# Performance work log

Measured on AMD Instinct MI355X. Metric: run time of the kernel, lower is better.

Reference implementation:

```python
import jax, jax.numpy as jnp
import numpy as np

# --- config (matches init_kwargs) ---
D_MODEL = 512
N_HEADS = 8
DIM_HEAD = D_MODEL // N_HEADS  # 64
BUCKET_SIZE = 64
N_HASHES = 4
B = 4
N = 4096
SELF_ATTN_VALUE = -5e4  # TOKEN_SELF_ATTN_VALUE in reformer_pytorch


def setup_inputs() -> dict:
    key = jax.random.key(0)
    ks = jax.random.split(key, 8)
    n_buckets = N // BUCKET_SIZE
    dh = N_HEADS * DIM_HEAD
    return {
        "queries": jax.random.normal(ks[0], (B, N, D_MODEL), jnp.float32),
        "keys": jax.random.normal(ks[1], (B, N, D_MODEL), jnp.float32),      # unused by module
        "values": jax.random.normal(ks[2], (B, N, D_MODEL), jnp.float32),    # unused by module
        "W_qk": jax.random.normal(ks[3], (D_MODEL, dh), jnp.float32) / np.float32(np.sqrt(D_MODEL)),
        "W_v": jax.random.normal(ks[4], (D_MODEL, dh), jnp.float32) / np.float32(np.sqrt(D_MODEL)),
        "W_out": jax.random.normal(ks[5], (dh, D_MODEL), jnp.float32) / np.float32(np.sqrt(dh)),
        "b_out": jnp.zeros((D_MODEL,), jnp.float32),
        # random LSH rotations: generated fresh (non-learnable) in torch; fixed here for determinism
        "rotations": jax.random.normal(ks[6], (DIM_HEAD, N_HASHES, n_buckets // 2), jnp.float32),
    }


def _look_one_back(x):
    # concat each chunk with the previous chunk along the within-chunk axis
    return jnp.concatenate([x, jnp.roll(x, 1, axis=1)], axis=2)


def lsh_attention(qk, v, rotations):
    # qk, v: (BH, T, dh) shared-QK LSH attention (reformer_pytorch LSHAttention)
    bh, T, dh = qk.shape
    n_buckets = T // BUCKET_SIZE
    total = N_HASHES * T

    # --- hash_vectors: random rotations + argmax over [R, -R] ---
    rotated = jnp.einsum('btf,fhi->bhti', qk, rotations)          # (bh, n_hashes, T, nb/2)
    rotated = jnp.concatenate([rotated, -rotated], axis=-1)       # (bh, n_hashes, T, nb)
    buckets = jnp.argmax(rotated, axis=-1)                        # (bh, n_hashes, T)
    offsets = (jnp.arange(N_HASHES) * n_buckets)[None, :, None]
    buckets = (buckets + offsets).reshape(bh, total)

    # --- stable sort by (bucket, position); keys are unique ---
    ticker = jnp.broadcast_to(jnp.arange(total)[None, :], (bh, total))
    buckets_and_t = T * buckets + (ticker % T)
    sticker = jnp.argsort(buckets_and_t, axis=-1)                 # (bh, total)
    undo_sort = jnp.argsort(sticker, axis=-1)
    st = sticker % T                                              # original positions, sorted

    sqk = jnp.take_along_axis(qk, st[:, :, None], axis=1)         # (bh, total, dh)
    sv = jnp.take_along_axis(v, st[:, :, None], axis=1)

    # --- chunk into bins; attend within chunk + one chunk back ---
    chunks = N_HASHES * n_buckets                                 # per-chunk len == BUCKET_SIZE
    bq_t = st.reshape(bh, chunks, -1)
    bqk = sqk.reshape(bh, chunks, -1, dh)
    bv = sv.reshape(bh, chunks, -1, dh)

    bq = bqk
    bk = bqk / jnp.maximum(jnp.linalg.norm(bqk, axis=-1, keepdims=True), 1e-12)  # F.normalize

    bk = _look_one_back(bk)       # (bh, chunks, 2*bs, dh)
    bv = _look_one_back(bv)
    bkv_t = _look_one_back(bq_t)  # (bh, chunks, 2*bs)

    dots = jnp.einsum('bcie,bcje->bcij', bq, bk) * (dh ** -0.5)   # (bh, chunks, bs, 2*bs)
    self_mask = bq_t[:, :, :, None] == bkv_t[:, :, None, :]
    dots = jnp.where(self_mask, SELF_ATTN_VALUE, dots)

    lse = jax.scipy.special.logsumexp(dots, axis=-1, keepdims=True)
    probs = jnp.exp(dots - lse)
    bo = jnp.einsum('bcij,bcje->bcie', probs, bv)                 # (bh, chunks, bs, dh)

    so = bo.reshape(bh, total, dh)
    slogits = lse.reshape(bh, total)
    o = jnp.take_along_axis(so, undo_sort[:, :, None], axis=1)
    logits = jnp.take_along_axis(slogits, undo_sort, axis=1)

    o = o.reshape(bh, N_HASHES, T, dh)
    logits = logits.reshape(bh, N_HASHES, T, 1)
    # combine hash rounds by softmax over per-round logsumexps
    w = jnp.exp(logits - jax.scipy.special.logsumexp(logits, axis=1, keepdims=True))
    return jnp.sum(o * w, axis=1)                                 # (bh, T, dh)


def reference(queries, keys, values, W_qk, W_v, W_out, b_out, rotations):
    Bsz, T, _ = queries.shape
    qk = queries @ W_qk                                           # (B, T, H*dh), no bias
    v = queries @ W_v

    def merge(x):
        return x.reshape(Bsz, T, N_HEADS, DIM_HEAD).transpose(0, 2, 1, 3).reshape(Bsz * N_HEADS, T, DIM_HEAD)

    out = lsh_attention(merge(qk), merge(v), rotations)           # (B*H, T, dh)
    out = out.reshape(Bsz, N_HEADS, T, DIM_HEAD).transpose(0, 2, 1, 3).reshape(Bsz, T, N_HEADS * DIM_HEAD)
    return out @ W_out + b_out                                    # to_out (with bias)
```

## Files before the change

### kernel.cpp

```cpp
#include <hip/hip_runtime.h>

typedef unsigned int uint32;
typedef _Float16 f16;
typedef _Float16 f16x8 __attribute__((ext_vector_type(8)));
typedef float f32x4 __attribute__((ext_vector_type(4)));

#define B_SZ 4
#define T_SZ 4096
#define DMODEL 512
#define NHEAD 8
#define DH 64
#define NHASH 4
#define BH (B_SZ*NHEAD)
#define NBUCK 256
#define TOT (NHASH*T_SZ)
#define M_TOK (B_SZ*T_SZ)

#define KSTRIDE 72
#define PSTRIDE 136

#define AMB_TAU 1.5e-3f

__global__ void k0_zero(int* hist, int* amb_cnt){
  hist[blockIdx.x*256 + threadIdx.x] = 0;
  if (blockIdx.x == 0 && threadIdx.x == 0) *amb_cnt = 0;
}

__global__ __launch_bounds__(256) void kw_t(const float* __restrict__ Wqk,
    const float* __restrict__ Wv, const float* __restrict__ Wout,
    f16* __restrict__ Wth, f16* __restrict__ Wtl)
{
  int gid = blockIdx.x*256 + threadIdx.x;
  int n = gid >> 9, k = gid & 511;
  int sel = n >> 9, col = n & 511;
  const float* src = (sel==0)? Wqk : (sel==1)? Wv : Wout;
  float v = src[(size_t)k*512 + col];
  f16 h = (f16)v;
  Wth[gid] = h;
  Wtl[gid] = (f16)(v - (float)h);
}

__global__ __launch_bounds__(256) void kr_t(const float* __restrict__ rot,
    f16* __restrict__ rotTh, f16* __restrict__ rotTl)
{
  int gid = blockIdx.x*256 + threadIdx.x;
  int n = gid >> 6, dd = gid & 63;
  float v = rot[dd*128 + n];
  f16 h = (f16)v;
  rotTh[gid] = h;
  rotTl[gid] = (f16)(v - (float)h);
}

__global__ __launch_bounds__(256) void k1a_split(const float* __restrict__ qin,
    f16* __restrict__ Ah, f16* __restrict__ Al)
{
  size_t gid = (size_t)blockIdx.x*256 + threadIdx.x;
  const float4* src = (const float4*)(qin) + gid*2;
  float4 x0 = src[0], x1 = src[1];
  float v[8] = {x0.x,x0.y,x0.z,x0.w, x1.x,x1.y,x1.z,x1.w};
  f16x8 h, l;
  #pragma unroll
  for (int e=0;e<8;e++){ f16 hh=(f16)v[e]; h[e]=hh; l[e]=(f16)(v[e]-(float)hh); }
  ((f16x8*)Ah)[gid] = h;
  ((f16x8*)Al)[gid] = l;
}

__global__ __launch_bounds__(256) void g_qkv(const f16* __restrict__ Ah,
    const f16* __restrict__ Al, const f16* __restrict__ Wth, const f16* __restrict__ Wtl,
    f16* __restrict__ qk16, f16* __restrict__ qkl, f16* __restrict__ v16)
{
  __shared__ f16 ah[128*KSTRIDE], al[128*KSTRIDE], bh[128*KSTRIDE], bl[128*KSTRIDE];
  int tid = threadIdx.x;
  int m0 = blockIdx.x*128, n0 = blockIdx.y*128;
  int w = tid >> 6, lane = tid & 63;
  int wm = w >> 1, wn = w & 1;
  int c_lane = lane & 15, quad = lane >> 4;

  f32x4 acc[4][4];
  #pragma unroll
  for (int mi=0;mi<4;mi++)
    #pragma unroll
    for (int ni=0;ni<4;ni++) acc[mi][ni] = (f32x4){0.f,0.f,0.f,0.f};

  int sr = tid >> 1, sc = (tid & 1) * 32;
  for (int kc=0; kc<8; kc++){
    int k0 = kc*64;
    {
      const f16x8* pah = (const f16x8*)(Ah + (size_t)(m0+sr)*512 + k0 + sc);
      const f16x8* pal = (const f16x8*)(Al + (size_t)(m0+sr)*512 + k0 + sc);
      const f16x8* pbh = (const f16x8*)(Wth + (size_t)(n0+sr)*512 + k0 + sc);
      const f16x8* pbl = (const f16x8*)(Wtl + (size_t)(n0+sr)*512 + k0 + sc);
      f16x8* dah = (f16x8*)&ah[sr*KSTRIDE + sc];
      f16x8* dal = (f16x8*)&al[sr*KSTRIDE + sc];
      f16x8* dbh = (f16x8*)&bh[sr*KSTRIDE + sc];
      f16x8* dbl = (f16x8*)&bl[sr*KSTRIDE + sc];
      #pragma unroll
      for (int i=0;i<4;i++){ dah[i]=pah[i]; dal[i]=pal[i]; dbh[i]=pbh[i]; dbl[i]=pbl[i]; }
    }
    __syncthreads();
    f16x8 fah[4][2], fal[4][2], fbh[4][2], fbl[4][2];
    #pragma unroll
    for (int i=0;i<4;i++)
      #pragma unroll
      for (int kb=0;kb<2;kb++){
        int ma = (wm*64 + i*16 + c_lane)*KSTRIDE + kb*32 + quad*8;
        int nb = (wn*64 + i*16 + c_lane)*KSTRIDE + kb*32 + quad*8;
        fah[i][kb] = *(const f16x8*)&ah[ma];
        fal[i][kb] = *(const f16x8*)&al[ma];
        fbh[i][kb] = *(const f16x8*)&bh[nb];
        fbl[i][kb] = *(const f16x8*)&bl[nb];
      }
    #pragma unroll
    for (int kb=0;kb<2;kb++)
      #pragma unroll
      for (int p=0;p<3;p++)
        #pragma unroll
        for (int mi=0;mi<4;mi++)
          #pragma unroll
          for (int ni=0;ni<4;ni++){
            f16x8 a = (p==2)? fal[mi][kb] : fah[mi][kb];
            f16x8 b = (p==1)? fbl[ni][kb] : fbh[ni][kb];
            acc[mi][ni] = __builtin_amdgcn_mfma_f32_16x16x32_f16(a, b, acc[mi][ni], 0,0,0);
          }
    __syncthreads();
  }

  #pragma unroll
  for (int mi=0;mi<4;mi++)
    #pragma unroll
    for (int ni=0;ni<4;ni++)
      #pragma unroll
      for (int r=0;r<4;r++){
        int n = n0 + wn*64 + ni*16 + c_lane;
        int tok = m0 + wm*64 + mi*16 + quad*4 + r;
        float val = acc[mi][ni][r];
        int b = tok >> 12, tp = tok & 4095;
        if (n < 512){
          int head = n >> 6, dd = n & 63;
          size_t idx = ((size_t)(b*NHEAD+head)*T_SZ + tp)*DH + dd;
          f16 hv = (f16)val;
          qk16[idx] = hv;
          qkl[idx]  = (f16)(val - (float)hv);
        } else {
          int j = n - 512, head = j >> 6, dd = j & 63;
          size_t idx = ((size_t)(b*NHEAD+head)*T_SZ + tp)*DH + dd;
          v16[idx] = (f16)val;
        }
      }
}

__global__ __launch_bounds__(256) void g_out(const f16* __restrict__ Xh,
    const f16* __restrict__ Xl, const f16* __restrict__ Wth, const f16* __restrict__ Wtl,
    const float* __restrict__ bout, float* __restrict__ out)
{
  __shared__ f16 ah[128*KSTRIDE], al[128*KSTRIDE], bh[128*KSTRIDE], bl[128*KSTRIDE];
  int tid = threadIdx.x;
  int m0 = blockIdx.x*128, n0 = blockIdx.y*128;
  int w = tid >> 6, lane = tid & 63;
  int wm = w >> 1, wn = w & 1;
  int c_lane = lane & 15, quad = lane >> 4;
  const f16* Bh_base = Wth + (size_t)1024*512;
  const f16* Bl_base = Wtl + (size_t)1024*512;

  f32x4 acc[4][4];
  #pragma unroll
  for (int mi=0;mi<4;mi++)
    #pragma unroll
    for (int ni=0;ni<4;ni++) acc[mi][ni] = (f32x4){0.f,0.f,0.f,0.f};

  int sr = tid >> 1, sc = (tid & 1) * 32;
  for (int kc=0; kc<8; kc++){
    int k0 = kc*64;
    {
      const f16x8* pah = (const f16x8*)(Xh + (size_t)(m0+sr)*512 + k0 + sc);
      const f16x8* pal = (const f16x8*)(Xl + (size_t)(m0+sr)*512 + k0 + sc);
      const f16x8* pbh = (const f16x8*)(Bh_base + (size_t)(n0+sr)*512 + k0 + sc);
      const f16x8* pbl = (const f16x8*)(Bl_base + (size_t)(n0+sr)*512 + k0 + sc);
      f16x8* dah = (f16x8*)&ah[sr*KSTRIDE + sc];
      f16x8* dal = (f16x8*)&al[sr*KSTRIDE + sc];
      f16x8* dbh = (f16x8*)&bh[sr*KSTRIDE + sc];
      f16x8* dbl = (f16x8*)&bl[sr*KSTRIDE + sc];
      #pragma unroll
      for (int i=0;i<4;i++){ dah[i]=pah[i]; dal[i]=pal[i]; dbh[i]=pbh[i]; dbl[i]=pbl[i]; }
    }
    __syncthreads();
    f16x8 fah[4][2], fal[4][2], fbh[4][2], fbl[4][2];
    #pragma unroll
    for (int i=0;i<4;i++)
      #pragma unroll
      for (int kb=0;kb<2;kb++){
        int ma = (wm*64 + i*16 + c_lane)*KSTRIDE + kb*32 + quad*8;
        int nb = (wn*64 + i*16 + c_lane)*KSTRIDE + kb*32 + quad*8;
        fah[i][kb] = *(const f16x8*)&ah[ma];
        fal[i][kb] = *(const f16x8*)&al[ma];
        fbh[i][kb] = *(const f16x8*)&bh[nb];
        fbl[i][kb] = *(const f16x8*)&bl[nb];
      }
    #pragma unroll
    for (int kb=0;kb<2;kb++)
      #pragma unroll
      for (int p=0;p<3;p++)
        #pragma unroll
        for (int mi=0;mi<4;mi++)
          #pragma unroll
          for (int ni=0;ni<4;ni++){
            f16x8 a = (p==2)? fal[mi][kb] : fah[mi][kb];
            f16x8 b = (p==1)? fbl[ni][kb] : fbh[ni][kb];
            acc[mi][ni] = __builtin_amdgcn_mfma_f32_16x16x32_f16(a, b, acc[mi][ni], 0,0,0);
          }
    __syncthreads();
  }

  #pragma unroll
  for (int mi=0;mi<4;mi++)
    #pragma unroll
    for (int ni=0;ni<4;ni++){
      int n = n0 + wn*64 + ni*16 + c_lane;
      float bn = bout[n];
      #pragma unroll
      for (int r=0;r<4;r++){
        int tok = m0 + wm*64 + mi*16 + quad*4 + r;
        out[(size_t)tok*512 + n] = acc[mi][ni][r] + bn;
      }
    }
}

__global__ __launch_bounds__(256) void k2_mfma(const f16* __restrict__ qkh,
    const f16* __restrict__ qkl, const f16* __restrict__ rotTh, const f16* __restrict__ rotTl,
    unsigned short* __restrict__ bucket, int* __restrict__ hist,
    int* __restrict__ amb_list, int* __restrict__ amb_cnt)
{
  int tid = threadIdx.x;
  int w = tid >> 6, lane = tid & 63;
  int wm = w >> 1, wn = w & 1;
  int c_lane = lane & 15, quad = lane >> 4;
  size_t m0 = (size_t)blockIdx.x*128 + wm*64;

  f16x8 fbh[4][2], fbl[4][2];
  #pragma unroll
  for (int ni=0;ni<4;ni++)
    #pragma unroll
    for (int kb=0;kb<2;kb++){
      int n = wn*64 + ni*16 + c_lane;
      fbh[ni][kb] = *(const f16x8*)&rotTh[n*64 + kb*32 + quad*8];
      fbl[ni][kb] = *(const f16x8*)&rotTl[n*64 + kb*32 + quad*8];
    }

  f32x4 acc[4][4];
  #pragma unroll
  for (int mi=0;mi<4;mi++)
    #pragma unroll
    for (int ni=0;ni<4;ni++) acc[mi][ni] = (f32x4){0.f,0.f,0.f,0.f};

  #pragma unroll
  for (int mi=0;mi<4;mi++){
    size_t row = m0 + mi*16 + c_lane;
    f16x8 fah[2], fal[2];
    #pragma unroll
    for (int kb=0;kb<2;kb++){
      fah[kb] = *(const f16x8*)&qkh[row*64 + kb*32 + quad*8];
      fal[kb] = *(const f16x8*)&qkl[row*64 + kb*32 + quad*8];
    }
    #pragma unroll
    for (int kb=0;kb<2;kb++)
      #pragma unroll
      for (int ni=0;ni<4;ni++){
        acc[mi][ni] = __builtin_amdgcn_mfma_f32_16x16x32_f16(fah[kb], fbh[ni][kb], acc[mi][ni], 0,0,0);
        acc[mi][ni] = __builtin_amdgcn_mfma_f32_16x16x32_f16(fah[kb], fbl[ni][kb], acc[mi][ni], 0,0,0);
        acc[mi][ni] = __builtin_amdgcn_mfma_f32_16x16x32_f16(fal[kb], fbh[ni][kb], acc[mi][ni], 0,0,0);
      }
  }

  #pragma unroll
  for (int mi=0;mi<4;mi++){
    #pragma unroll
    for (int r=0;r<4;r++){
      int tok = (int)m0 + mi*16 + quad*4 + r;
      int bhh = tok >> 12, t = tok & 4095;
      #pragma unroll
      for (int hl=0; hl<2; hl++){
        int h = wn*2 + hl;
        float v0 = acc[mi][2*hl][r];
        float v1 = acc[mi][2*hl+1][r];
        float m1 = v0, m2 = -1e30f; int b1 = c_lane;
        if (v1 > m1){ m2 = m1; m1 = v1; b1 = 16 + c_lane; } else m2 = v1;
        float n0v = -v0, n1v = -v1;
        if (n0v > m1){ m2 = m1; m1 = n0v; b1 = 32 + c_lane; } else if (n0v > m2) m2 = n0v;
        if (n1v > m1){ m2 = m1; m1 = n1v; b1 = 48 + c_lane; } else if (n1v > m2) m2 = n1v;
        float ssq = v0*v0 + v1*v1;
        #pragma unroll
        for (int d2=1; d2<16; d2<<=1){
          float om1 = __shfl_xor(m1, d2);
          float om2 = __shfl_xor(m2, d2);
          int   ob1 = __shfl_xor(b1, d2);
          ssq += __shfl_xor(ssq, d2);
          if (om1 > m1){ m2 = fmaxf(m1, om2); m1 = om1; b1 = ob1; }
          else         { m2 = fmaxf(m2, om1); }
        }
        if (c_lane == 0){
          float rms = sqrtf(ssq * (1.0f/32.0f));
          if (m1 - m2 < AMB_TAU * rms){
            int idx = atomicAdd(amb_cnt, 1);
            amb_list[idx] = (bhh<<14) | (h<<12) | t;
          } else {
            int g = b1 + (h<<6);
            bucket[((bhh*NHASH + h)<<12) + t] = (unsigned short)g;
            atomicAdd(&hist[bhh*NBUCK + g], 1);
          }
        }
      }
    }
  }
}

__global__ __launch_bounds__(64) void k2_fix(const float* __restrict__ qin,
    const float* __restrict__ Wqk, const float* __restrict__ rot,
    const int* __restrict__ amb_list, const int* __restrict__ amb_cnt,
    unsigned short* __restrict__ bucket, int* __restrict__ hist)
{
  __shared__ __align__(16) float qs[512];
  __shared__ double qk64[64];
  __shared__ double accs[32];
  int n = *amb_cnt;
  int lane = threadIdx.x;
  for (int it = blockIdx.x; it < n; it += gridDim.x){
    int gid = amb_list[it];
    int t = gid & (T_SZ-1);
    int h = (gid >> 12) & 3;
    int bh = gid >> 14;
    int b = bh >> 3, head = bh & 7;
    const float4* qrow4 = (const float4*)(qin + ((size_t)b*T_SZ + t)*DMODEL);
    float4 x0 = qrow4[lane];
    float4 x1 = qrow4[lane + 64];
    *(float4*)&qs[lane*4]       = x0;
    *(float4*)&qs[256 + lane*4] = x1;
    __syncthreads();
    const float* wcol = Wqk + head*64 + lane;
    double s = 0.0;
    #pragma unroll 16
    for (int d=0; d<512; d++)
      s += (double)qs[d] * (double)wcol[(size_t)d*512];
    qk64[lane] = s;
    __syncthreads();
    if (lane < 32){
      double a = 0.0;
      #pragma unroll 16
      for (int f=0; f<64; f++)
        a += qk64[f] * (double)rot[f*(NHASH*32) + h*32 + lane];
      accs[lane] = a;
    }
    __syncthreads();
    if (lane == 0){
      double best = accs[0]; int bk = 0;
      for (int k=1;k<64;k++){
        double vv = (k<32)? accs[k] : -accs[k-32];
        if (vv > best){ best = vv; bk = k; }
      }
      int g = bk + (h<<6);
      bucket[((bh*NHASH + h)<<12) + t] = (unsigned short)g;
      atomicAdd(&hist[bh*NBUCK + g], 1);
    }
    __syncthreads();
  }
}

__global__ __launch_bounds__(256) void k3_scan(const int* __restrict__ hist, int* __restrict__ starts){
  __shared__ int s[256];
  int bh = blockIdx.x, tid = threadIdx.x;
  int v = hist[bh*256 + tid];
  s[tid] = v; __syncthreads();
  for (int off=1; off<256; off<<=1){
    int a = (tid >= off) ? s[tid-off] : 0;
    __syncthreads();
    s[tid] += a;
    __syncthreads();
  }
  starts[bh*256 + tid] = s[tid] - v;
}

__global__ __launch_bounds__(64) void k3b_scatter(const unsigned short* __restrict__ bucket,
    const int* __restrict__ starts, int* __restrict__ st)
{
  int blk = blockIdx.x;
  int bh = blk >> 8; int g = blk & 255; int h = g >> 6;
  int lane = threadIdx.x;
  const unsigned short* brow = bucket + ((bh*NHASH + h)<<12);
  int base = starts[bh*NBUCK + g];
  for (int step=0; step<64; step++){
    int t = step*64 + lane;
    bool pred = (brow[t] == (unsigned short)g);
    unsigned long long mask = __ballot(pred);
    if (pred){
      int off = __popcll(mask & ((1ull<<lane) - 1ull));
      st[bh*TOT + base + off] = t;
    }
    base += __popcll(mask);
  }
}

__global__ __launch_bounds__(256, 4) void k4_attn(const f16* __restrict__ qk16,
    const f16* __restrict__ v16, const int* __restrict__ st,
    float* __restrict__ lse_out, f16* __restrict__ o_out)
{
  __shared__ __align__(16) char smem[36864];
  f16*   k_lds   = (f16*)smem;
  f16*   p_lds   = (f16*)smem;
  f16*   vT      = (f16*)(smem + 18432);
  float* invnorm = (float*)(smem + 35840);
  int*   kv_t    = (int*)(smem + 36352);

  int bid = blockIdx.x;
  int swz = (bid & 7) * 1024 + (bid >> 3);
  int bh = swz >> 8; int c = swz & 255;
  int h = c >> 6; int cp = (c + 255) & 255;
  int tid = threadIdx.x;
  int w = tid >> 6, lane = tid & 63;
  int c_lane = lane & 15, quad = lane >> 4;
  const int* strow = st + bh*TOT;

  if (tid < 128){
    int row = tid;
    int slot = (row < 64) ? (c*64 + row) : (cp*64 + row - 64);
    int t = strow[slot];
    kv_t[row] = t;
    const f16x8* kr = (const f16x8*)(qk16 + ((size_t)bh*T_SZ + t)*DH);
    const f16x8* vr = (const f16x8*)(v16  + ((size_t)bh*T_SZ + t)*DH);
    f16x8 kv[8], vv[8];
    float ss = 0.f;
    #pragma unroll
    for (int i=0;i<8;i++){
      f16x8 x = kr[i]; kv[i] = x;
      vv[i] = vr[i];
      #pragma unroll
      for (int e=0;e<8;e++){ float f = (float)x[e]; ss += f*f; }
    }
    invnorm[row] = 1.0f / fmaxf(sqrtf(ss), 1e-12f);
    f16x8* kd = (f16x8*)&k_lds[row*KSTRIDE];
    #pragma unroll
    for (int i=0;i<8;i++) kd[i] = kv[i];
    #pragma unroll
    for (int i=0;i<8;i++){
      #pragma unroll
      for (int e=0;e<8;e++) vT[(i*8+e)*PSTRIDE + row] = vv[i][e];
    }
  }
  __syncthreads();

  int mi = w;
  f16x8 aq[2];
  #pragma unroll
  for (int kb=0;kb<2;kb++)
    aq[kb] = *(const f16x8*)&k_lds[(mi*16 + c_lane)*KSTRIDE + kb*32 + quad*8];

  f32x4 accS[8];
  #pragma unroll
  for (int ni=0;ni<8;ni++) accS[ni] = (f32x4){0.f,0.f,0.f,0.f};

  #pragma unroll
  for (int ni=0;ni<8;ni++){
    int rowb = ni*16 + c_lane;
    f16 sc = (f16)invnorm[rowb];
    f16x8 b0 = *(const f16x8*)&k_lds[rowb*KSTRIDE + 0*32 + quad*8];
    f16x8 b1 = *(const f16x8*)&k_lds[rowb*KSTRIDE + 1*32 + quad*8];
    b0 *= sc; b1 *= sc;
    accS[ni] = __builtin_amdgcn_mfma_f32_16x16x32_f16(aq[0], b0, accS[ni], 0,0,0);
    accS[ni] = __builtin_amdgcn_mfma_f32_16x16x32_f16(aq[1], b1, accS[ni], 0,0,0);
  }

  int tq[4];
  #pragma unroll
  for (int r=0;r<4;r++) tq[r] = kv_t[mi*16 + quad*4 + r];
  int tk[8];
  #pragma unroll
  for (int ni=0;ni<8;ni++) tk[ni] = kv_t[ni*16 + c_lane];

  float mrow[4], lrow[4];
  #pragma unroll
  for (int r=0;r<4;r++){
    float mx = -1e30f;
    #pragma unroll
    for (int ni=0;ni<8;ni++){
      float s = accS[ni][r] * 0.125f;
      if (tk[ni] == tq[r]) s = -50000.0f;
      accS[ni][r] = s;
      mx = fmaxf(mx, s);
    }
    mx = fmaxf(mx, __shfl_xor(mx, 1));
    mx = fmaxf(mx, __shfl_xor(mx, 2));
    mx = fmaxf(mx, __shfl_xor(mx, 4));
    mx = fmaxf(mx, __shfl_xor(mx, 8));
    mrow[r] = mx;
    float ls = 0.f;
    #pragma unroll
    for (int ni=0;ni<8;ni++){
      float e = __expf(accS[ni][r] - mx);
      accS[ni][r] = e;
      ls += e;
    }
    ls += __shfl_xor(ls, 1);
    ls += __shfl_xor(ls, 2);
    ls += __shfl_xor(ls, 4);
    ls += __shfl_xor(ls, 8);
    lrow[r] = ls;
  }

  __syncthreads();

  #pragma unroll
  for (int ni=0;ni<8;ni++)
    #pragma unroll
    for (int r=0;r<4;r++)
      p_lds[(mi*16 + quad*4 + r)*PSTRIDE + ni*16 + c_lane] = (f16)accS[ni][r];

  f16x8 pa[4];
  #pragma unroll
  for (int kb=0;kb<4;kb++)
    pa[kb] = *(const f16x8*)&p_lds[(mi*16 + c_lane)*PSTRIDE + kb*32 + quad*8];

  size_t rowbase = (size_t)(bh*NHASH + h)*T_SZ;
  #pragma unroll
  for (int ni2=0;ni2<4;ni2++){
    f16x8 bv[4];
    #pragma unroll
    for (int kb=0;kb<4;kb++)
      bv[kb] = *(const f16x8*)&vT[(ni2*16 + c_lane)*PSTRIDE + kb*32 + quad*8];
    f32x4 accO = (f32x4){0.f,0.f,0.f,0.f};
    #pragma unroll
    for (int kb=0;kb<4;kb++)
      accO = __builtin_amdgcn_mfma_f32_16x16x32_f16(pa[kb], bv[kb], accO, 0,0,0);
    #pragma unroll
    for (int r=0;r<4;r++){
      float invl = 1.0f / lrow[r];
      f16* orow = o_out + (rowbase + tq[r])*DH;
      orow[ni2*16 + c_lane] = (f16)(accO[r] * invl);
    }
  }
  #pragma unroll
  for (int r=0;r<4;r++){
    if (c_lane == 0)
      lse_out[rowbase + tq[r]] = mrow[r] + logf(lrow[r]);
  }
}

__global__ __launch_bounds__(256) void k5_comb(const float* __restrict__ lse,
    const f16* __restrict__ o_f16, f16* __restrict__ Xh, f16* __restrict__ Xl)
{
  int gid = blockIdx.x*256 + threadIdx.x;
  int t = gid & (T_SZ-1);
  int bh = gid >> 12;
  size_t base = (size_t)bh*NHASH*T_SZ + t;
  float l0 = lse[base];
  float l1 = lse[base + T_SZ];
  float l2 = lse[base + 2*T_SZ];
  float l3 = lse[base + 3*T_SZ];
  float M = fmaxf(fmaxf(l0,l1), fmaxf(l2,l3));
  float e0 = __expf(l0-M), e1 = __expf(l1-M), e2 = __expf(l2-M), e3 = __expf(l3-M);
  float inv = 1.0f/(e0+e1+e2+e3);
  float w0=e0*inv, w1=e1*inv, w2=e2*inv, w3=e3*inv;
  const f16x8* r0 = (const f16x8*)(o_f16 + base*DH);
  const f16x8* r1 = (const f16x8*)(o_f16 + (base + (size_t)T_SZ)*DH);
  const f16x8* r2 = (const f16x8*)(o_f16 + (base + (size_t)2*T_SZ)*DH);
  const f16x8* r3 = (const f16x8*)(o_f16 + (base + (size_t)3*T_SZ)*DH);
  int b = bh >> 3, head = bh & 7;
  size_t xofs = ((size_t)(b*T_SZ + t)*DMODEL + head*DH);
  f16x8* xh = (f16x8*)(Xh + xofs);
  f16x8* xl = (f16x8*)(Xl + xofs);
  #pragma unroll
  for (int i=0; i<8; i++){
    f16x8 a = r0[i], bb = r1[i], cc = r2[i], dd = r3[i];
    f16x8 ho, lo;
    #pragma unroll
    for (int e=0;e<8;e++){
      float res = w0*(float)a[e] + w1*(float)bb[e] + w2*(float)cc[e] + w3*(float)dd[e];
      f16 hh = (f16)res;
      ho[e] = hh; lo[e] = (f16)(res - (float)hh);
    }
    xh[i] = ho; xl[i] = lo;
  }
}

extern "C" void kernel_launch(void* const* d_in, const int* in_sizes, int n_in,
                              void* d_out, int out_size, void* d_ws, size_t ws_size,
                              hipStream_t stream) {
  const float* queries = (const float*)d_in[0];
  const float* Wqk     = (const float*)d_in[3];
  const float* Wv      = (const float*)d_in[4];
  const float* Wout    = (const float*)d_in[5];
  const float* bout    = (const float*)d_in[6];
  const float* rot     = (const float*)d_in[7];
  float* out = (float*)d_out;

  const size_t SZ_F16  = (size_t)BH*T_SZ*DH*2;
  const size_t SZ_WT   = (size_t)1536*512*2;
  const size_t SZ_ROT  = (size_t)128*64*2;
  const size_t SZ_O    = (size_t)BH*NHASH*T_SZ*DH*2;
  const size_t OFS_X      = 0;
  const size_t OFS_AH     = OFS_X    + 2*SZ_F16;
  const size_t OFS_AL     = OFS_AH   + SZ_F16;
  const size_t OFS_QK16   = OFS_AL   + SZ_F16;
  const size_t OFS_V16    = OFS_QK16 + SZ_F16;
  const size_t OFS_WTH    = OFS_V16  + SZ_F16;
  const size_t OFS_WTL    = OFS_WTH  + SZ_WT;
  const size_t OFS_ROTH   = OFS_WTL  + SZ_WT;
  const size_t OFS_ROTL   = OFS_ROTH + SZ_ROT;
  const size_t OFS_O      = OFS_ROTL + SZ_ROT;
  const size_t OFS_BUCKET = OFS_O    + SZ_O;
  const size_t OFS_HIST   = OFS_BUCKET + (size_t)BH*NHASH*T_SZ*2;
  const size_t OFS_STARTS = OFS_HIST   + (size_t)BH*NBUCK*4;
  const size_t OFS_ST     = OFS_STARTS + (size_t)BH*NBUCK*4;
  const size_t OFS_LSE    = OFS_ST     + (size_t)BH*TOT*4;
  const size_t OFS_AMB    = OFS_LSE    + (size_t)BH*NHASH*T_SZ*4;
  const size_t OFS_CNT    = OFS_AMB    + (size_t)BH*NHASH*T_SZ*4;
  const size_t WS_NEEDED  = OFS_CNT    + 256;
  if (ws_size < WS_NEEDED) return;

  char* ws = (char*)d_ws;
  f16*      qkl    = (f16*)(ws + OFS_X);
  f16*      Xh     = (f16*)(ws + OFS_X);
  f16*      Xl     = (f16*)(ws + OFS_X + SZ_F16);
  f16*      Ah     = (f16*)(ws + OFS_AH);
  f16*      Al     = (f16*)(ws + OFS_AL);
  f16*      qk16   = (f16*)(ws + OFS_QK16);
  f16*      v16    = (f16*)(ws + OFS_V16);
  f16*      Wth    = (f16*)(ws + OFS_WTH);
  f16*      Wtl    = (f16*)(ws + OFS_WTL);
  f16*      rotTh  = (f16*)(ws + OFS_ROTH);
  f16*      rotTl  = (f16*)(ws + OFS_ROTL);
  f16*      o_f16  = (f16*)(ws + OFS_O);
  unsigned short* bucket = (unsigned short*)(ws + OFS_BUCKET);
  int*      hist   = (int*)(ws + OFS_HIST);
  int*      starts = (int*)(ws + OFS_STARTS);
  int*      st     = (int*)(ws + OFS_ST);
  float*    lse    = (float*)(ws + OFS_LSE);
  int*      amb    = (int*)(ws + OFS_AMB);
  int*      cnt    = (int*)(ws + OFS_CNT);

  k0_zero   <<<BH, 256, 0, stream>>>(hist, cnt);
  kw_t      <<<(1536*512)/256, 256, 0, stream>>>(Wqk, Wv, Wout, Wth, Wtl);
  kr_t      <<<(128*64)/256, 256, 0, stream>>>(rot, rotTh, rotTl);
  k1a_split <<<(M_TOK*DMODEL/8)/256, 256, 0, stream>>>(queries, Ah, Al);
  g_qkv     <<<dim3(M_TOK/128, 8), 256, 0, stream>>>(Ah, Al, Wth, Wtl, qk16, qkl, v16);
  k2_mfma   <<<(BH*T_SZ)/128, 256, 0, stream>>>(qk16, qkl, rotTh, rotTl, bucket, hist, amb, cnt);
  k2_fix    <<<2048, 64, 0, stream>>>(queries, Wqk, rot, amb, cnt, bucket, hist);
  k3_scan   <<<BH, 256, 0, stream>>>(hist, starts);
  k3b_scatter<<<BH*NBUCK, 64, 0, stream>>>(bucket, starts, st);
  k4_attn   <<<BH*256, 256, 0, stream>>>(qk16, v16, st, lse, o_f16);
  k5_comb   <<<(BH*T_SZ)/256, 256, 0, stream>>>(lse, o_f16, Xh, Xl);
  g_out     <<<dim3(M_TOK/128, 4), 256, 0, stream>>>(Xh, Xl, Wth, Wtl, bout, out);
}
```

Baseline: 526.0 us.

## Build bucket histogram in scan kernel and transpose hash MFMA layout

The global atomic bucket histogram is removed from the hashing and fix-up kernels. The scan kernel now rebuilds each head's histogram from the bucket array using shared-memory atomics. The hashing MFMA is transposed so each wave handles 16 tokens across all 128 rotation columns, putting the argmax mostly in registers with only two cross-quad shuffles. The aim is to cut global atomic contention and shuffle work, at the cost of re-reading the bucket array in the scan kernel.

```diff
diff --git a/kernel.cpp b/kernel.cpp
--- a/kernel.cpp
+++ b/kernel.cpp
@@ -4,6 +4,7 @@
 typedef _Float16 f16;
 typedef _Float16 f16x8 __attribute__((ext_vector_type(8)));
 typedef float f32x4 __attribute__((ext_vector_type(4)));
+typedef unsigned short u16x8 __attribute__((ext_vector_type(8)));
 
 #define B_SZ 4
 #define T_SZ 4096
@@ -21,9 +22,8 @@
 
 #define AMB_TAU 1.5e-3f
 
-__global__ void k0_zero(int* hist, int* amb_cnt){
-  hist[blockIdx.x*256 + threadIdx.x] = 0;
-  if (blockIdx.x == 0 && threadIdx.x == 0) *amb_cnt = 0;
+__global__ void k0_zero(int* amb_cnt){
+  if (threadIdx.x == 0 && blockIdx.x == 0) *amb_cnt = 0;
 }
 
 __global__ __launch_bounds__(256) void kw_t(const float* __restrict__ Wqk,
@@ -225,89 +225,72 @@
     }
 }
 
-__global__ __launch_bounds__(256) void k2_mfma(const f16* __restrict__ qkh,
+__global__ __launch_bounds__(256, 4) void k2_mfma(const f16* __restrict__ qkh,
     const f16* __restrict__ qkl, const f16* __restrict__ rotTh, const f16* __restrict__ rotTl,
-    unsigned short* __restrict__ bucket, int* __restrict__ hist,
+    unsigned short* __restrict__ bucket,
     int* __restrict__ amb_list, int* __restrict__ amb_cnt)
 {
   int tid = threadIdx.x;
   int w = tid >> 6, lane = tid & 63;
-  int wm = w >> 1, wn = w & 1;
   int c_lane = lane & 15, quad = lane >> 4;
-  size_t m0 = (size_t)blockIdx.x*128 + wm*64;
-
-  f16x8 fbh[4][2], fbl[4][2];
-  #pragma unroll
-  for (int ni=0;ni<4;ni++)
+  int tok0 = (blockIdx.x*4 + w)*16;
+  size_t rowb = (size_t)(tok0 + c_lane)*64;
+
+  f16x8 tbh[2], tbl[2];
+  #pragma unroll
+  for (int kb=0;kb<2;kb++){
+    tbh[kb] = *(const f16x8*)&qkh[rowb + kb*32 + quad*8];
+    tbl[kb] = *(const f16x8*)&qkl[rowb + kb*32 + quad*8];
+  }
+
+  f32x4 acc[8];
+  #pragma unroll
+  for (int mi=0;mi<8;mi++) acc[mi] = (f32x4){0.f,0.f,0.f,0.f};
+
+  #pragma unroll
+  for (int mi=0;mi<8;mi++){
+    int aoff = (mi*16 + c_lane)*64;
     #pragma unroll
     for (int kb=0;kb<2;kb++){
-      int n = wn*64 + ni*16 + c_lane;
-      fbh[ni][kb] = *(const f16x8*)&rotTh[n*64 + kb*32 + quad*8];
-      fbl[ni][kb] = *(const f16x8*)&rotTl[n*64 + kb*32 + quad*8];
-    }
-
-  f32x4 acc[4][4];
-  #pragma unroll
-  for (int mi=0;mi<4;mi++)
-    #pragma unroll
-    for (int ni=0;ni<4;ni++) acc[mi][ni] = (f32x4){0.f,0.f,0.f,0.f};
-
-  #pragma unroll
-  for (int mi=0;mi<4;mi++){
-    size_t row = m0 + mi*16 + c_lane;
-    f16x8 fah[2], fal[2];
-    #pragma unroll
-    for (int kb=0;kb<2;kb++){
-      fah[kb] = *(const f16x8*)&qkh[row*64 + kb*32 + quad*8];
-      fal[kb] = *(const f16x8*)&qkl[row*64 + kb*32 + quad*8];
-    }
-    #pragma unroll
-    for (int kb=0;kb<2;kb++)
-      #pragma unroll
-      for (int ni=0;ni<4;ni++){
-        acc[mi][ni] = __builtin_amdgcn_mfma_f32_16x16x32_f16(fah[kb], fbh[ni][kb], acc[mi][ni], 0,0,0);
-        acc[mi][ni] = __builtin_amdgcn_mfma_f32_16x16x32_f16(fah[kb], fbl[ni][kb], acc[mi][ni], 0,0,0);
-        acc[mi][ni] = __builtin_amdgcn_mfma_f32_16x16x32_f16(fal[kb], fbh[ni][kb], acc[mi][ni], 0,0,0);
-      }
-  }
-
-  #pragma unroll
-  for (int mi=0;mi<4;mi++){
-    #pragma unroll
-    for (int r=0;r<4;r++){
-      int tok = (int)m0 + mi*16 + quad*4 + r;
-      int bhh = tok >> 12, t = tok & 4095;
-      #pragma unroll
-      for (int hl=0; hl<2; hl++){
-        int h = wn*2 + hl;
-        float v0 = acc[mi][2*hl][r];
-        float v1 = acc[mi][2*hl+1][r];
-        float m1 = v0, m2 = -1e30f; int b1 = c_lane;
-        if (v1 > m1){ m2 = m1; m1 = v1; b1 = 16 + c_lane; } else m2 = v1;
-        float n0v = -v0, n1v = -v1;
-        if (n0v > m1){ m2 = m1; m1 = n0v; b1 = 32 + c_lane; } else if (n0v > m2) m2 = n0v;
-        if (n1v > m1){ m2 = m1; m1 = n1v; b1 = 48 + c_lane; } else if (n1v > m2) m2 = n1v;
-        float ssq = v0*v0 + v1*v1;
-        #pragma unroll
-        for (int d2=1; d2<16; d2<<=1){
-          float om1 = __shfl_xor(m1, d2);
-          float om2 = __shfl_xor(m2, d2);
-          int   ob1 = __shfl_xor(b1, d2);
-          ssq += __shfl_xor(ssq, d2);
-          if (om1 > m1){ m2 = fmaxf(m1, om2); m1 = om1; b1 = ob1; }
-          else         { m2 = fmaxf(m2, om1); }
-        }
-        if (c_lane == 0){
-          float rms = sqrtf(ssq * (1.0f/32.0f));
-          if (m1 - m2 < AMB_TAU * rms){
-            int idx = atomicAdd(amb_cnt, 1);
-            amb_list[idx] = (bhh<<14) | (h<<12) | t;
-          } else {
-            int g = b1 + (h<<6);
-            bucket[((bhh*NHASH + h)<<12) + t] = (unsigned short)g;
-            atomicAdd(&hist[bhh*NBUCK + g], 1);
-          }
-        }
+      f16x8 arh = *(const f16x8*)&rotTh[aoff + kb*32 + quad*8];
+      f16x8 arl = *(const f16x8*)&rotTl[aoff + kb*32 + quad*8];
+      acc[mi] = __builtin_amdgcn_mfma_f32_16x16x32_f16(arh, tbh[kb], acc[mi], 0,0,0);
+      acc[mi] = __builtin_amdgcn_mfma_f32_16x16x32_f16(arl, tbh[kb], acc[mi], 0,0,0);
+      acc[mi] = __builtin_amdgcn_mfma_f32_16x16x32_f16(arh, tbl[kb], acc[mi], 0,0,0);
+    }
+  }
+
+  int tokg = tok0 + c_lane;
+  int bhh = tokg >> 12, t = tokg & 4095;
+
+  #pragma unroll
+  for (int h=0; h<4; h++){
+    float m1 = -1e30f, m2 = -1e30f, ssq = 0.f; int b1 = 0;
+    #pragma unroll
+    for (int u=0; u<8; u++){
+      float v = acc[2*h + (u>>2)][u&3];
+      int bidd = (u>>2)*16 + quad*4 + (u&3);
+      ssq += v*v;
+      if (v > m1){ m2=m1; m1=v; b1=bidd; } else if (v > m2) m2=v;
+      float nv = -v;
+      if (nv > m1){ m2=m1; m1=nv; b1=bidd+32; } else if (nv > m2) m2=nv;
+    }
+    #pragma unroll
+    for (int d2=16; d2<64; d2<<=1){
+      float om1 = __shfl_xor(m1, d2);
+      float om2 = __shfl_xor(m2, d2);
+      int   ob1 = __shfl_xor(b1, d2);
+      ssq += __shfl_xor(ssq, d2);
+      if (om1 > m1){ m2 = fmaxf(m1, om2); m1 = om1; b1 = ob1; }
+      else          { m2 = fmaxf(m2, om1); }
+    }
+    if (quad == 0){
+      float rms = sqrtf(ssq * (1.0f/32.0f));
+      if (m1 - m2 < AMB_TAU * rms){
+        int idx = atomicAdd(amb_cnt, 1);
+        amb_list[idx] = (bhh<<14) | (h<<12) | t;
+      } else {
+        bucket[((bhh*NHASH + h)<<12) + t] = (unsigned short)(b1 + (h<<6));
       }
     }
   }
@@ -316,7 +299,7 @@
 __global__ __launch_bounds__(64) void k2_fix(const float* __restrict__ qin,
     const float* __restrict__ Wqk, const float* __restrict__ rot,
     const int* __restrict__ amb_list, const int* __restrict__ amb_cnt,
-    unsigned short* __restrict__ bucket, int* __restrict__ hist)
+    unsigned short* __restrict__ bucket)
 {
   __shared__ __align__(16) float qs[512];
   __shared__ double qk64[64];
@@ -358,17 +341,26 @@
       }
       int g = bk + (h<<6);
       bucket[((bh*NHASH + h)<<12) + t] = (unsigned short)g;
-      atomicAdd(&hist[bh*NBUCK + g], 1);
-    }
-    __syncthreads();
-  }
-}
-
-__global__ __launch_bounds__(256) void k3_scan(const int* __restrict__ hist, int* __restrict__ starts){
+    }
+    __syncthreads();
+  }
+}
+
+__global__ __launch_bounds__(256) void k3_scan(const unsigned short* __restrict__ bucket,
+    int* __restrict__ starts){
   __shared__ int s[256];
   int bh = blockIdx.x, tid = threadIdx.x;
-  int v = hist[bh*256 + tid];
-  s[tid] = v; __syncthreads();
+  s[tid] = 0;
+  __syncthreads();
+  const u16x8* b8 = (const u16x8*)(bucket + ((size_t)bh*NHASH << 12));
+  for (int i = tid; i < 2048; i += 256){
+    u16x8 x = b8[i];
+    #pragma unroll
+    for (int e=0;e<8;e++) atomicAdd(&s[x[e]], 1);
+  }
+  __syncthreads();
+  int v = s[tid];
+  __syncthreads();
   for (int off=1; off<256; off<<=1){
     int a = (tid >= off) ? s[tid-off] : 0;
     __syncthreads();
@@ -628,21 +620,20 @@
   f16*      rotTl  = (f16*)(ws + OFS_ROTL);
   f16*      o_f16  = (f16*)(ws + OFS_O);
   unsigned short* bucket = (unsigned short*)(ws + OFS_BUCKET);
-  int*      hist   = (int*)(ws + OFS_HIST);
   int*      starts = (int*)(ws + OFS_STARTS);
   int*      st     = (int*)(ws + OFS_ST);
   float*    lse    = (float*)(ws + OFS_LSE);
   int*      amb    = (int*)(ws + OFS_AMB);
   int*      cnt    = (int*)(ws + OFS_CNT);
 
-  k0_zero   <<<BH, 256, 0, stream>>>(hist, cnt);
+  k0_zero   <<<1, 64, 0, stream>>>(cnt);
   kw_t      <<<(1536*512)/256, 256, 0, stream>>>(Wqk, Wv, Wout, Wth, Wtl);
   kr_t      <<<(128*64)/256, 256, 0, stream>>>(rot, rotTh, rotTl);
   k1a_split <<<(M_TOK*DMODEL/8)/256, 256, 0, stream>>>(queries, Ah, Al);
   g_qkv     <<<dim3(M_TOK/128, 8), 256, 0, stream>>>(Ah, Al, Wth, Wtl, qk16, qkl, v16);
-  k2_mfma   <<<(BH*T_SZ)/128, 256, 0, stream>>>(qk16, qkl, rotTh, rotTl, bucket, hist, amb, cnt);
-  k2_fix    <<<2048, 64, 0, stream>>>(queries, Wqk, rot, amb, cnt, bucket, hist);
-  k3_scan   <<<BH, 256, 0, stream>>>(hist, starts);
+  k2_mfma   <<<(BH*T_SZ)/64, 256, 0, stream>>>(qk16, qkl, rotTh, rotTl, bucket, amb, cnt);
+  k2_fix    <<<2048, 64, 0, stream>>>(queries, Wqk, rot, amb, cnt, bucket);
+  k3_scan   <<<BH, 256, 0, stream>>>(bucket, starts);
   k3b_scatter<<<BH*NBUCK, 64, 0, stream>>>(bucket, starts, st);
   k4_attn   <<<BH*256, 256, 0, stream>>>(qk16, v16, st, lse, o_f16);
   k5_comb   <<<(BH*T_SZ)/256, 256, 0, stream>>>(lse, o_f16, Xh, Xl);
```

Result: faster. 491.5 us (-6.6%).
